# Kernel tuning notes

Hardware: AMD Instinct MI355X
Metric: run time of the kernel (lower is better)

## Reference

```python
import jax, jax.numpy as jnp
import numpy as np

B, S, H, NH, L, V, P = 2, 1024, 768, 12, 4, 32000, 1024
HD = H // NH  # head dim = 64; matches scale_val = hidden/num_heads


def setup_inputs() -> dict:
    key = jax.random.key(0)
    ks = jax.random.split(key, 18)
    sc = 0.02
    n = jax.random.normal
    return {
        "input_ids": jax.random.randint(ks[0], (B, S), 0, V, dtype=jnp.int32),
        "seq_mask": jnp.ones((B, S), jnp.float32),
        "bpe_emb": (n(ks[1], (V, H)) * sc).astype(jnp.float32),
        "pos_emb": (n(ks[2], (P, H)) * sc).astype(jnp.float32),
        "qkv_w": (n(ks[3], (L, H, 3 * H)) * sc).astype(jnp.float32),
        "qkv_b": jnp.zeros((L, 3 * H), jnp.float32),
        "res_w": (n(ks[4], (L, H, H)) * sc).astype(jnp.float32),
        "res_b": jnp.zeros((L, H), jnp.float32),
        "ln1_g": jnp.ones((L, H), jnp.float32),
        "ln1_b": jnp.zeros((L, H), jnp.float32),
        "ff1_w": (n(ks[5], (L, H, 4 * H)) * sc).astype(jnp.float32),
        "ff1_b": jnp.zeros((L, 4 * H), jnp.float32),
        "ff2_w": (n(ks[6], (L, 4 * H, H)) * sc).astype(jnp.float32),
        "ff2_b": jnp.zeros((L, H), jnp.float32),
        "ln2_g": jnp.ones((L, H), jnp.float32),
        "ln2_b": jnp.zeros((L, H), jnp.float32),
        "pred_w": (n(ks[7], (H, V)) * sc).astype(jnp.float32),
    }


def _layer_norm(x, g, b, e=1e-5):
    u = jnp.mean(x, -1, keepdims=True)
    s = jnp.mean((x - u) ** 2, -1, keepdims=True)
    return g * ((x - u) / jnp.sqrt(s + e)) + b


def _attention(x, seq_mask, w_qkv, b_qkv, w_res, b_res):
    qkv = x @ w_qkv + b_qkv                    # [B,S,3H]
    q, k, v = jnp.split(qkv, 3, axis=-1)
    q = q.reshape(B, S, NH, HD)
    k = k.reshape(B, S, NH, HD)
    v = v.reshape(B, S, NH, HD)
    score = jnp.einsum('bqhd,bkhd->bhqk', q, k) / jnp.sqrt(jnp.float32(HD))
    tril = jnp.tril(jnp.ones((S, S), jnp.float32))           # causal
    mask = tril[None, None] * seq_mask[:, None, None, :]      # [B,1,S,S]
    score = score + (1.0 - mask) * -1e9
    prob = jax.nn.softmax(score, axis=-1)      # dropout rate 0 -> identity
    val = jnp.einsum('bhqk,bkhd->bqhd', prob, v).reshape(B, S, H)
    return val @ w_res + b_res                 # dropout rate 0 -> identity


def reference(input_ids, seq_mask, bpe_emb, pos_emb, qkv_w, qkv_b, res_w, res_b,
              ln1_g, ln1_b, ff1_w, ff1_b, ff2_w, ff2_b, ln2_g, ln2_b, pred_w):
    pos_idx = jnp.arange(S)
    h = bpe_emb[input_ids] + pos_emb[pos_idx][None]           # [B,S,H]
    for l in range(L):
        a = _attention(h, seq_mask, qkv_w[l], qkv_b[l], res_w[l], res_b[l])
        h = _layer_norm(h + a, ln1_g[l], ln1_b[l])
        m = (jax.nn.gelu(h @ ff1_w[l] + ff1_b[l], approximate=False)
             @ ff2_w[l] + ff2_b[l])
        h = _layer_norm(h + m, ln2_g[l], ln2_b[l])
    pred_score = h @ pred_w                                   # [B,S,V]
    pred_prob = jax.nn.softmax(pred_score, axis=-1)
    return pred_score, pred_prob
```

## Files before the change

kernel.cpp:

```cpp
#include <hip/hip_runtime.h>
#include <math.h>

#define BB 2
#define SS 1024
#define HH 768
#define NHEAD 12
#define HDIM 64
#define NLAYER 4
#define VV 32000
#define MROWS (BB*SS)

typedef unsigned short u16;
typedef __attribute__((ext_vector_type(8))) short short8;
typedef __attribute__((ext_vector_type(4))) float f32x4;
typedef __attribute__((ext_vector_type(4))) unsigned short u16x4;

__device__ __forceinline__ u16 f2bf(float f) {
    union { float f; unsigned u; } x; x.f = f;
    unsigned r = (x.u + 0x7fff + ((x.u >> 16) & 1)) >> 16;
    return (u16)r;
}
__device__ __forceinline__ float bf2f(u16 b) {
    union { unsigned u; float f; } x; x.u = ((unsigned)b) << 16;
    return x.f;
}

__device__ __forceinline__ void gload_lds16(const u16* g, u16* l) {
    __builtin_amdgcn_global_load_lds((const __attribute__((address_space(1))) void*)g,
                                     (__attribute__((address_space(3))) void*)l, 16, 0, 0);
}

__global__ __launch_bounds__(256) void conv_all(
    const float* __restrict__ qkv_w, u16* __restrict__ qkvT,
    const float* __restrict__ res_w, u16* __restrict__ resT,
    const float* __restrict__ ff1_w, u16* __restrict__ ff1T,
    const float* __restrict__ ff2_w, u16* __restrict__ ff2T,
    const float* __restrict__ pred_w, u16* __restrict__ predT) {
    int id = blockIdx.x;
    const float* W; u16* Wt; int K, N, rem;
    if (id < 6912) {
        int l = id / 1728; rem = id - l * 1728;
        W = qkv_w + (size_t)l * HH * 3 * HH; Wt = qkvT + (size_t)l * HH * 3 * HH;
        K = HH; N = 3 * HH;
    } else if (id < 9216) {
        id -= 6912; int l = id / 576; rem = id - l * 576;
        W = res_w + (size_t)l * HH * HH; Wt = resT + (size_t)l * HH * HH;
        K = HH; N = HH;
    } else if (id < 18432) {
        id -= 9216; int l = id / 2304; rem = id - l * 2304;
        W = ff1_w + (size_t)l * HH * 4 * HH; Wt = ff1T + (size_t)l * HH * 4 * HH;
        K = HH; N = 4 * HH;
    } else if (id < 27648) {
        id -= 18432; int l = id / 2304; rem = id - l * 2304;
        W = ff2_w + (size_t)l * 4 * HH * HH; Wt = ff2T + (size_t)l * 4 * HH * HH;
        K = 4 * HH; N = HH;
    } else {
        rem = id - 27648;
        W = pred_w; Wt = predT; K = HH; N = VV;
    }
    const int nt = N / 32;
    const int k0 = (rem / nt) * 32, n0 = (rem % nt) * 32;

    __shared__ u16 tile[32][33];
    int t = threadIdx.x;
    int ky = t >> 3, nx = (t & 7) * 4;
    float4 v = *(const float4*)(W + (size_t)(k0 + ky) * N + n0 + nx);
    tile[nx + 0][ky] = f2bf(v.x);
    tile[nx + 1][ky] = f2bf(v.y);
    tile[nx + 2][ky] = f2bf(v.z);
    tile[nx + 3][ky] = f2bf(v.w);
    __syncthreads();
    int nr = t >> 3, kc = (t & 7) * 4;
    u16x4 o;
    o[0] = tile[nr][kc + 0]; o[1] = tile[nr][kc + 1];
    o[2] = tile[nr][kc + 2]; o[3] = tile[nr][kc + 3];
    *(u16x4*)(Wt + (size_t)(n0 + nr) * K + k0 + kc) = o;
}

__global__ void embed_kernel(const int* __restrict__ ids,
                             const float* __restrict__ bpe,
                             const float* __restrict__ pos,
                             float* __restrict__ h, u16* __restrict__ hb) {
    int row = blockIdx.x;
    int s = row % SS;
    int id = ids[row];
    const float4* br = (const float4*)(bpe + (size_t)id * HH);
    const float4* pr = (const float4*)(pos + (size_t)s * HH);
    float4* hr = (float4*)(h + (size_t)row * HH);
    u16x4* hbr = (u16x4*)(hb + (size_t)row * HH);
    int t = threadIdx.x;
    float4 a = br[t], c = pr[t];
    a.x += c.x; a.y += c.y; a.z += c.z; a.w += c.w;
    hr[t] = a;
    u16x4 u; u[0] = f2bf(a.x); u[1] = f2bf(a.y); u[2] = f2bf(a.z); u[3] = f2bf(a.w);
    hbr[t] = u;
}

template<int BM, int THREADS, int WN, int ACT, int WF32, int WBF>
__global__ __launch_bounds__(THREADS) void mfma_gemm(
    const u16* __restrict__ A, const u16* __restrict__ Wt,
    const float* __restrict__ bias, float* __restrict__ C,
    u16* __restrict__ Cb, int M, int N, int K) {
    constexpr int WM = THREADS / 64 / WN;
    constexpr int MR = BM / (WM * 16);
    constexpr int NR = 128 / (WN * 16);
    constexpr int LPT = (BM * 8 + 1024) / THREADS;
    __shared__ u16 As[2 * BM * 64];
    __shared__ u16 Bs[2 * 128 * 64];
    const int tid = threadIdx.x;
    const int lane = tid & 63;
    const int wid = tid >> 6;

    const int nwg = gridDim.x * gridDim.y;
    int id = blockIdx.x + gridDim.x * blockIdx.y;
    int id2 = (nwg & 7) ? id : ((id & 7) * (nwg >> 3) + (id >> 3));
    const int brow = (id2 % gridDim.x) * BM;
    const int bcol = (id2 / gridDim.x) * 128;

    const int wr = (wid / WN) * (MR * 16);
    const int wc = (wid % WN) * (NR * 16);
    f32x4 acc[MR][NR] = {};

    const u16* Abase = A + (size_t)brow * K;
    const u16* Bbase = Wt + (size_t)bcol * K;
    const int lrow = lane & 15;
    const int lhi = lane >> 4;

    auto stage = [&](u16* Ad, u16* Bd, int kt) {
#pragma unroll
        for (int c0 = 0; c0 < BM * 8; c0 += THREADS) {
            int c = c0 + tid;
            int r = c >> 3, s = c & 7;
            gload_lds16(Abase + (size_t)r * K + kt + ((s ^ (r & 7)) * 8), Ad + c * 8);
        }
#pragma unroll
        for (int c0 = 0; c0 < 1024; c0 += THREADS) {
            int c = c0 + tid;
            int r = c >> 3, s = c & 7;
            gload_lds16(Bbase + (size_t)r * K + kt + ((s ^ (r & 7)) * 8), Bd + c * 8);
        }
    };

    const int nt = K / 64;
    stage(As, Bs, 0);
    for (int t = 0; t < nt; ++t) {
        u16* Ac = As + (t & 1) * (BM * 64);
        u16* Bc = Bs + (t & 1) * (128 * 64);
        if (t + 1 < nt) {
            stage(As + ((t + 1) & 1) * (BM * 64),
                  Bs + ((t + 1) & 1) * (128 * 64), (t + 1) * 64);
            if constexpr (LPT == 8)      asm volatile("s_waitcnt vmcnt(8)" ::: "memory");
            else if constexpr (LPT == 6) asm volatile("s_waitcnt vmcnt(6)" ::: "memory");
            else if constexpr (LPT == 5) asm volatile("s_waitcnt vmcnt(5)" ::: "memory");
            else                         asm volatile("s_waitcnt vmcnt(4)" ::: "memory");
        } else {
            asm volatile("s_waitcnt vmcnt(0)" ::: "memory");
        }
        __builtin_amdgcn_s_barrier();
        __builtin_amdgcn_sched_barrier(0);

        short8 a[MR][2], b[NR][2];
#pragma unroll
        for (int m = 0; m < MR; ++m) {
            const int R = wr + m * 16 + lrow;
            char* rp = (char*)Ac + R * 128;
#pragma unroll
            for (int kk = 0; kk < 2; ++kk)
                a[m][kk] = *(const short8*)(rp + (((kk * 4 + lhi) ^ (R & 7)) * 16));
        }
#pragma unroll
        for (int n = 0; n < NR; ++n) {
            const int R = wc + n * 16 + lrow;
            char* rp = (char*)Bc + R * 128;
#pragma unroll
            for (int kk = 0; kk < 2; ++kk)
                b[n][kk] = *(const short8*)(rp + (((kk * 4 + lhi) ^ (R & 7)) * 16));
        }
        __builtin_amdgcn_s_setprio(1);
#pragma unroll
        for (int kk = 0; kk < 2; ++kk)
#pragma unroll
            for (int m = 0; m < MR; ++m)
#pragma unroll
                for (int n = 0; n < NR; ++n)
                    acc[m][n] = __builtin_amdgcn_mfma_f32_16x16x32_bf16(a[m][kk], b[n][kk], acc[m][n], 0, 0, 0);
        __builtin_amdgcn_s_setprio(0);

        __builtin_amdgcn_sched_barrier(0);
        __builtin_amdgcn_s_barrier();
    }

    const int lr4 = (lane >> 4) * 4;
#pragma unroll
    for (int n = 0; n < NR; ++n) {
        int col = bcol + wc + n * 16 + lrow;
        float bv = bias ? bias[col] : 0.f;
#pragma unroll
        for (int m = 0; m < MR; ++m) {
#pragma unroll
            for (int j = 0; j < 4; ++j) {
                int row = brow + wr + m * 16 + lr4 + j;
                float v = acc[m][n][j] + bv;
                if (ACT == 1) v = 0.5f * v * (1.f + erff(v * 0.70710678118654752f));
                if (WF32) C[(size_t)row * N + col] = v;
                if (WBF)  Cb[(size_t)row * N + col] = f2bf(v);
            }
        }
    }
}

__global__ __launch_bounds__(256) void attn_kernel(
    const u16* __restrict__ qkvb, const float* __restrict__ seq_mask,
    u16* __restrict__ av) {
    __shared__ u16 Ks[128 * 64];
    __shared__ u16 Vt[64 * 128];
    __shared__ u16 Ps[64 * 128];
    const int qb = gridDim.x - 1 - blockIdx.x;
    const int hd = blockIdx.y, b = blockIdx.z;
    const int t = threadIdx.x;
    const int lane = t & 63;
    const int w = t >> 6;
    const int lrow = lane & 15;
    const int lhi = lane >> 4;
    const int q0 = qb * 64;
    const size_t rs = 3 * HH;

    short8 aq[2];
    {
        const u16* qrow = qkvb + (size_t)(b * SS + q0 + w * 16 + lrow) * rs + hd * HDIM;
        aq[0] = *(const short8*)(qrow + lhi * 8);
        aq[1] = *(const short8*)(qrow + 32 + lhi * 8);
    }

    f32x4 o[4] = {};
    float m_[4] = {-INFINITY, -INFINITY, -INFINITY, -INFINITY};
    float l_[4] = {0.f, 0.f, 0.f, 0.f};

    const int kr = t >> 1;
    const int ch = t & 1;
    const int ntile = (q0 + 64 + 127) / 128;

    short8 kR[4], vR[4];
    {
        const u16* kbase = qkvb + (size_t)(b * SS + kr) * rs + HH + hd * HDIM + ch * 32;
#pragma unroll
        for (int i = 0; i < 4; ++i) {
            kR[i] = *(const short8*)(kbase + i * 8);
            vR[i] = *(const short8*)(kbase + HH + i * 8);
        }
    }

    for (int kt = 0; kt < ntile; ++kt) {
        const int k0 = kt * 128;
        __syncthreads();
        {
            char* kp = (char*)Ks + kr * 128;
#pragma unroll
            for (int i = 0; i < 4; ++i)
                *(short8*)(kp + (((ch * 4 + i) ^ (kr & 7)) << 4)) = kR[i];
            const int vslot = kr >> 3;
            const int voff = (kr & 7) * 2;
#pragma unroll
            for (int i = 0; i < 4; ++i)
#pragma unroll
                for (int e = 0; e < 8; ++e) {
                    int d = ch * 32 + i * 8 + e;
                    *(u16*)((char*)Vt + d * 256 + ((vslot ^ (d & 15)) << 4) + voff) = (u16)vR[i][e];
                }
        }
        __syncthreads();

        if (kt + 1 < ntile) {
            const u16* kbase = qkvb + (size_t)(b * SS + k0 + 128 + kr) * rs + HH + hd * HDIM + ch * 32;
#pragma unroll
            for (int i = 0; i < 4; ++i) {
                kR[i] = *(const short8*)(kbase + i * 8);
                vR[i] = *(const short8*)(kbase + HH + i * 8);
            }
        }

        f32x4 s[8] = {};
        __builtin_amdgcn_s_setprio(1);
#pragma unroll
        for (int n = 0; n < 8; ++n) {
            const int krow = n * 16 + lrow;
            char* kp = (char*)Ks + krow * 128;
#pragma unroll
            for (int c = 0; c < 2; ++c) {
                short8 bk = *(const short8*)(kp + (((c * 4 + lhi) ^ (krow & 7)) << 4));
                s[n] = __builtin_amdgcn_mfma_f32_16x16x32_bf16(aq[c], bk, s[n], 0, 0, 0);
            }
        }
        __builtin_amdgcn_s_setprio(0);

        float sm[8];
#pragma unroll
        for (int n = 0; n < 8; ++n) sm[n] = seq_mask[b * SS + k0 + n * 16 + lrow];
        const int diag = (kt == ntile - 1);
#pragma unroll
        for (int j = 0; j < 4; ++j) {
            const int qglob = q0 + w * 16 + lhi * 4 + j;
            float sv[8];
#pragma unroll
            for (int n = 0; n < 8; ++n) {
                const int kglob = k0 + n * 16 + lrow;
                float msk = (diag && kglob > qglob) ? 0.f : sm[n];
                sv[n] = s[n][j] * 0.125f + (1.f - msk) * (-1e9f);
            }
            float tm = fmaxf(fmaxf(fmaxf(sv[0], sv[1]), fmaxf(sv[2], sv[3])),
                             fmaxf(fmaxf(sv[4], sv[5]), fmaxf(sv[6], sv[7])));
            tm = fmaxf(tm, __shfl_xor(tm, 1));
            tm = fmaxf(tm, __shfl_xor(tm, 2));
            tm = fmaxf(tm, __shfl_xor(tm, 4));
            tm = fmaxf(tm, __shfl_xor(tm, 8));
            float mn = fmaxf(m_[j], tm);
            float sc = __expf(m_[j] - mn);
            float ps = 0.f;
#pragma unroll
            for (int n = 0; n < 8; ++n) {
                float p = __expf(sv[n] - mn);
                s[n][j] = p;
                ps += p;
            }
            ps += __shfl_xor(ps, 1);
            ps += __shfl_xor(ps, 2);
            ps += __shfl_xor(ps, 4);
            ps += __shfl_xor(ps, 8);
            l_[j] = l_[j] * sc + ps;
            m_[j] = mn;
#pragma unroll
            for (int dn = 0; dn < 4; ++dn) o[dn][j] *= sc;
        }

#pragma unroll
        for (int j = 0; j < 4; ++j) {
            const int prow = w * 16 + lhi * 4 + j;
            char* pp = (char*)Ps + prow * 256;
            const int poff = (lrow & 7) * 2;
#pragma unroll
            for (int n = 0; n < 8; ++n) {
                int slot = 2 * n + (lrow >> 3);
                *(u16*)(pp + ((slot ^ (prow & 15)) << 4) + poff) = f2bf(s[n][j]);
            }
        }

        const int arow = w * 16 + lrow;
        char* ap_p = (char*)Ps + arow * 256;
        __builtin_amdgcn_s_setprio(1);
#pragma unroll
        for (int c = 0; c < 4; ++c) {
            short8 ap = *(const short8*)(ap_p + (((c * 4 + lhi) ^ (arow & 15)) << 4));
#pragma unroll
            for (int dn = 0; dn < 4; ++dn) {
                const int vrow = dn * 16 + lrow;
                short8 bv = *(const short8*)((char*)Vt + vrow * 256 +
                                             (((c * 4 + lhi) ^ (vrow & 15)) << 4));
                o[dn] = __builtin_amdgcn_mfma_f32_16x16x32_bf16(ap, bv, o[dn], 0, 0, 0);
            }
        }
        __builtin_amdgcn_s_setprio(0);
    }

#pragma unroll
    for (int j = 0; j < 4; ++j) {
        const int q = q0 + w * 16 + lhi * 4 + j;
        const float inv = 1.f / l_[j];
        u16* orow = av + (size_t)(b * SS + q) * HH + hd * HDIM;
#pragma unroll
        for (int dn = 0; dn < 4; ++dn)
            orow[dn * 16 + lrow] = f2bf(o[dn][j] * inv);
    }
}

__global__ __launch_bounds__(256) void add_ln_kernel(
    float* __restrict__ h, u16* __restrict__ hb,
    const u16* __restrict__ ab,
    const float* __restrict__ g, const float* __restrict__ bta) {
    const int row = blockIdx.x * 4 + (threadIdx.x >> 6);
    const int lane = threadIdx.x & 63;
    const size_t base = (size_t)row * HH;

    float x[12];
    float sum = 0.f;
#pragma unroll
    for (int c = 0; c < 3; ++c) {
        const int col = lane * 4 + c * 256;
        float4 hv = *(const float4*)(h + base + col);
        u16x4 av = *(const u16x4*)(ab + base + col);
        x[c*4+0] = hv.x + bf2f(av[0]);
        x[c*4+1] = hv.y + bf2f(av[1]);
        x[c*4+2] = hv.z + bf2f(av[2]);
        x[c*4+3] = hv.w + bf2f(av[3]);
        sum += x[c*4+0] + x[c*4+1] + x[c*4+2] + x[c*4+3];
    }
#pragma unroll
    for (int off = 32; off; off >>= 1) sum += __shfl_xor(sum, off);
    const float mean = sum * (1.0f / 768.0f);

    float vs = 0.f;
#pragma unroll
    for (int e = 0; e < 12; ++e) { float d = x[e] - mean; vs += d * d; }
#pragma unroll
    for (int off = 32; off; off >>= 1) vs += __shfl_xor(vs, off);
    const float inv = 1.0f / sqrtf(vs * (1.0f / 768.0f) + 1e-5f);

#pragma unroll
    for (int c = 0; c < 3; ++c) {
        const int col = lane * 4 + c * 256;
        float4 gv = *(const float4*)(g + col);
        float4 bv = *(const float4*)(bta + col);
        float y0 = gv.x * (x[c*4+0] - mean) * inv + bv.x;
        float y1 = gv.y * (x[c*4+1] - mean) * inv + bv.y;
        float y2 = gv.z * (x[c*4+2] - mean) * inv + bv.z;
        float y3 = gv.w * (x[c*4+3] - mean) * inv + bv.w;
        float4 hv; hv.x = y0; hv.y = y1; hv.z = y2; hv.w = y3;
        *(float4*)(h + base + col) = hv;
        u16x4 u; u[0] = f2bf(y0); u[1] = f2bf(y1); u[2] = f2bf(y2); u[3] = f2bf(y3);
        *(u16x4*)(hb + base + col) = u;
    }
}

__global__ __launch_bounds__(512) void softmax_v_kernel(
    const float* __restrict__ score, float* __restrict__ prob) {
    __shared__ u16 srow[VV];
    __shared__ float red[512];
    int row = blockIdx.x;
    int t = threadIdx.x;
    const float4* sr = (const float4*)(score + (size_t)row * VV);
    float4* pr = (float4*)(prob + (size_t)row * VV);
    const int n4 = VV / 4;

    float mx = -INFINITY;
    for (int i = t; i < n4; i += 512) {
        float4 v = sr[i];
        u16x4 u; u[0] = f2bf(v.x); u[1] = f2bf(v.y); u[2] = f2bf(v.z); u[3] = f2bf(v.w);
        *(u16x4*)(srow + i * 4) = u;
        mx = fmaxf(mx, fmaxf(fmaxf(bf2f(u[0]), bf2f(u[1])), fmaxf(bf2f(u[2]), bf2f(u[3]))));
    }
    red[t] = mx; __syncthreads();
    for (int o = 256; o; o >>= 1) { if (t < o) red[t] = fmaxf(red[t], red[t + o]); __syncthreads(); }
    mx = red[0];
    __syncthreads();

    float s = 0.f;
    for (int i = t; i < n4; i += 512) {
        u16x4 u = *(const u16x4*)(srow + i * 4);
        s += __expf(bf2f(u[0]) - mx) + __expf(bf2f(u[1]) - mx)
           + __expf(bf2f(u[2]) - mx) + __expf(bf2f(u[3]) - mx);
    }
    red[t] = s; __syncthreads();
    for (int o = 256; o; o >>= 1) { if (t < o) red[t] += red[t + o]; __syncthreads(); }
    float inv = 1.0f / red[0];

    for (int i = t; i < n4; i += 512) {
        u16x4 u = *(const u16x4*)(srow + i * 4);
        float4 o4;
        o4.x = __expf(bf2f(u[0]) - mx) * inv; o4.y = __expf(bf2f(u[1]) - mx) * inv;
        o4.z = __expf(bf2f(u[2]) - mx) * inv; o4.w = __expf(bf2f(u[3]) - mx) * inv;
        pr[i] = o4;
    }
}

extern "C" void kernel_launch(void* const* d_in, const int* in_sizes, int n_in,
                              void* d_out, int out_size, void* d_ws, size_t ws_size,
                              hipStream_t stream) {
    const int*   ids      = (const int*)d_in[0];
    const float* seq_mask = (const float*)d_in[1];
    const float* bpe      = (const float*)d_in[2];
    const float* pos      = (const float*)d_in[3];
    const float* qkv_w    = (const float*)d_in[4];
    const float* qkv_b    = (const float*)d_in[5];
    const float* res_w    = (const float*)d_in[6];
    const float* res_b    = (const float*)d_in[7];
    const float* ln1_g    = (const float*)d_in[8];
    const float* ln1_b    = (const float*)d_in[9];
    const float* ff1_w    = (const float*)d_in[10];
    const float* ff1_b    = (const float*)d_in[11];
    const float* ff2_w    = (const float*)d_in[12];
    const float* ff2_b    = (const float*)d_in[13];
    const float* ln2_g    = (const float*)d_in[14];
    const float* ln2_b    = (const float*)d_in[15];
    const float* pred_w   = (const float*)d_in[16];

    float* out_score = (float*)d_out;
    float* out_prob  = out_score + (size_t)MROWS * VV;

    size_t off = 0;
    auto take = [&](size_t bytes) -> size_t {
        size_t p = off; off += (bytes + 255) & ~(size_t)255; return p;
    };
    const size_t o_qkvT = take((size_t)NLAYER * HH * 3 * HH * 2);
    const size_t o_resT = take((size_t)NLAYER * HH * HH * 2);
    const size_t o_ff1T = take((size_t)NLAYER * HH * 4 * HH * 2);
    const size_t o_ff2T = take((size_t)NLAYER * 4 * HH * HH * 2);
    const size_t o_predT = take((size_t)HH * VV * 2);
    const size_t o_h    = take((size_t)MROWS * HH * 4);
    const size_t o_ab   = take((size_t)MROWS * HH * 2);
    const size_t o_qkvb = take((size_t)MROWS * 3 * HH * 2);
    const size_t o_hb   = take((size_t)MROWS * HH * 2);
    const size_t o_avb  = take((size_t)MROWS * HH * 2);
    const size_t o_midb = take((size_t)MROWS * 4 * HH * 2);
    const size_t need = off;

    char* arena = (ws_size >= need) ? (char*)d_ws : (char*)out_prob;
    u16*   qkvT = (u16*)(arena + o_qkvT);
    u16*   resT = (u16*)(arena + o_resT);
    u16*   ff1T = (u16*)(arena + o_ff1T);
    u16*   ff2T = (u16*)(arena + o_ff2T);
    u16*   predT = (u16*)(arena + o_predT);
    float* h    = (float*)(arena + o_h);
    u16*   ab   = (u16*)(arena + o_ab);
    u16*   qkvb = (u16*)(arena + o_qkvb);
    u16*   hb   = (u16*)(arena + o_hb);
    u16*   avb  = (u16*)(arena + o_avb);
    u16*   midb = (u16*)(arena + o_midb);

    conv_all<<<51648, 256, 0, stream>>>(qkv_w, qkvT, res_w, resT,
                                        ff1_w, ff1T, ff2_w, ff2T, pred_w, predT);

    embed_kernel<<<MROWS, 192, 0, stream>>>(ids, bpe, pos, h, hb);

    for (int l = 0; l < NLAYER; ++l) {
        mfma_gemm<64, 256, 2, 0, 0, 1><<<dim3(MROWS / 64, 3 * HH / 128), 256, 0, stream>>>(
            hb, qkvT + (size_t)l * HH * 3 * HH, qkv_b + (size_t)l * 3 * HH,
            nullptr, qkvb, MROWS, 3 * HH, HH);
        attn_kernel<<<dim3(SS / 64, NHEAD, BB), 256, 0, stream>>>(qkvb, seq_mask, avb);
        mfma_gemm<32, 256, 2, 0, 0, 1><<<dim3(MROWS / 32, HH / 128), 256, 0, stream>>>(
            avb, resT + (size_t)l * HH * HH, res_b + (size_t)l * HH,
            nullptr, ab, MROWS, HH, HH);
        add_ln_kernel<<<MROWS / 4, 256, 0, stream>>>(h, hb, ab,
            ln1_g + (size_t)l * HH, ln1_b + (size_t)l * HH);
        mfma_gemm<64, 256, 2, 1, 0, 1><<<dim3(MROWS / 64, 4 * HH / 128), 256, 0, stream>>>(
            hb, ff1T + (size_t)l * HH * 4 * HH, ff1_b + (size_t)l * 4 * HH,
            nullptr, midb, MROWS, 4 * HH, HH);
        mfma_gemm<32, 256, 2, 0, 0, 1><<<dim3(MROWS / 32, HH / 128), 256, 0, stream>>>(
            midb, ff2T + (size_t)l * 4 * HH * HH, ff2_b + (size_t)l * HH,
            nullptr, ab, MROWS, HH, 4 * HH);
        add_ln_kernel<<<MROWS / 4, 256, 0, stream>>>(h, hb, ab,
            ln2_g + (size_t)l * HH, ln2_b + (size_t)l * HH);
    }

    mfma_gemm<128, 512, 4, 0, 1, 0><<<dim3(MROWS / 128, VV / 128), 512, 0, stream>>>(
        hb, predT, nullptr, out_score, nullptr, MROWS, VV, HH);
    softmax_v_kernel<<<MROWS, 512, 0, stream>>>(out_score, out_prob);
}
```

Measured before the change: 933.9 us.

## Generalize GEMM to multi-stage pipeline with configurable K-tile depth

```diff
diff --git a/kernel.cpp b/kernel.cpp
--- a/kernel.cpp
+++ b/kernel.cpp
@@ -96,7 +96,7 @@
     hbr[t] = u;
 }
 
-template<int BM, int THREADS, int WN, int ACT, int WF32, int WBF>
+template<int BM, int BK, int NBUF, int THREADS, int WN, int ACT, int WF32, int WBF>
 __global__ __launch_bounds__(THREADS) void mfma_gemm(
     const u16* __restrict__ A, const u16* __restrict__ Wt,
     const float* __restrict__ bias, float* __restrict__ C,
@@ -104,9 +104,15 @@
     constexpr int WM = THREADS / 64 / WN;
     constexpr int MR = BM / (WM * 16);
     constexpr int NR = 128 / (WN * 16);
-    constexpr int LPT = (BM * 8 + 1024) / THREADS;
-    __shared__ u16 As[2 * BM * 64];
-    __shared__ u16 Bs[2 * 128 * 64];
+    constexpr int KK = BK / 32;
+    constexpr int SLOTS = BK / 8;
+    constexpr int SM = SLOTS - 1;
+    constexpr int RB = BK * 2;
+    constexpr int ACH = BM * BK / 8;
+    constexpr int BCH = 128 * BK / 8;
+    constexpr int LPT = (ACH + BCH) / THREADS;
+    __shared__ u16 As[NBUF * BM * BK];
+    __shared__ u16 Bs[NBUF * 128 * BK];
     const int tid = threadIdx.x;
     const int lane = tid & 63;
     const int wid = tid >> 6;
@@ -126,59 +132,72 @@
     const int lrow = lane & 15;
     const int lhi = lane >> 4;
 
-    auto stage = [&](u16* Ad, u16* Bd, int kt) {
-#pragma unroll
-        for (int c0 = 0; c0 < BM * 8; c0 += THREADS) {
+    auto stage = [&](int buf, int tile) {
+        const int kt = tile * BK;
+        u16* Ad = As + buf * (BM * BK);
+        u16* Bd = Bs + buf * (128 * BK);
+#pragma unroll
+        for (int c0 = 0; c0 < ACH; c0 += THREADS) {
             int c = c0 + tid;
-            int r = c >> 3, s = c & 7;
-            gload_lds16(Abase + (size_t)r * K + kt + ((s ^ (r & 7)) * 8), Ad + c * 8);
-        }
-#pragma unroll
-        for (int c0 = 0; c0 < 1024; c0 += THREADS) {
+            int r = c / SLOTS, s = c & SM;
+            gload_lds16(Abase + (size_t)r * K + kt + ((s ^ (r & SM)) * 8), Ad + c * 8);
+        }
+#pragma unroll
+        for (int c0 = 0; c0 < BCH; c0 += THREADS) {
             int c = c0 + tid;
-            int r = c >> 3, s = c & 7;
-            gload_lds16(Bbase + (size_t)r * K + kt + ((s ^ (r & 7)) * 8), Bd + c * 8);
+            int r = c / SLOTS, s = c & SM;
+            gload_lds16(Bbase + (size_t)r * K + kt + ((s ^ (r & SM)) * 8), Bd + c * 8);
         }
     };
 
-    const int nt = K / 64;
-    stage(As, Bs, 0);
+    const int nt = K / BK;
+#pragma unroll
+    for (int p = 0; p < NBUF - 1; ++p)
+        if (p < nt) stage(p, p);
+
     for (int t = 0; t < nt; ++t) {
-        u16* Ac = As + (t & 1) * (BM * 64);
-        u16* Bc = Bs + (t & 1) * (128 * 64);
-        if (t + 1 < nt) {
-            stage(As + ((t + 1) & 1) * (BM * 64),
-                  Bs + ((t + 1) & 1) * (128 * 64), (t + 1) * 64);
-            if constexpr (LPT == 8)      asm volatile("s_waitcnt vmcnt(8)" ::: "memory");
-            else if constexpr (LPT == 6) asm volatile("s_waitcnt vmcnt(6)" ::: "memory");
+        const int nf = t + NBUF - 1;
+        if (nf < nt) stage(nf % NBUF, nf);
+        const int rem = ((nf < nt) ? nf : (nt - 1)) - t;
+        if (rem <= 0) {
+            asm volatile("s_waitcnt vmcnt(0)" ::: "memory");
+        } else if (rem == 1) {
+            if constexpr (LPT == 3)      asm volatile("s_waitcnt vmcnt(3)" ::: "memory");
+            else if constexpr (LPT == 4) asm volatile("s_waitcnt vmcnt(4)" ::: "memory");
             else if constexpr (LPT == 5) asm volatile("s_waitcnt vmcnt(5)" ::: "memory");
-            else                         asm volatile("s_waitcnt vmcnt(4)" ::: "memory");
+            else                         asm volatile("s_waitcnt vmcnt(6)" ::: "memory");
+        } else if (rem == 2) {
+            if constexpr (LPT == 3)      asm volatile("s_waitcnt vmcnt(6)" ::: "memory");
+            else                         asm volatile("s_waitcnt vmcnt(12)" ::: "memory");
         } else {
-            asm volatile("s_waitcnt vmcnt(0)" ::: "memory");
+            if constexpr (LPT == 3)      asm volatile("s_waitcnt vmcnt(9)" ::: "memory");
+            else                         asm volatile("s_waitcnt vmcnt(18)" ::: "memory");
         }
         __builtin_amdgcn_s_barrier();
         __builtin_amdgcn_sched_barrier(0);
 
-        short8 a[MR][2], b[NR][2];
+        u16* Ac = As + (t % NBUF) * (BM * BK);
+        u16* Bc = Bs + (t % NBUF) * (128 * BK);
+        short8 a[MR][KK], b[NR][KK];
 #pragma unroll
         for (int m = 0; m < MR; ++m) {
             const int R = wr + m * 16 + lrow;
-            char* rp = (char*)Ac + R * 128;
-#pragma unroll
-            for (int kk = 0; kk < 2; ++kk)
-                a[m][kk] = *(const short8*)(rp + (((kk * 4 + lhi) ^ (R & 7)) * 16));
+            char* rp = (char*)Ac + R * RB;
+#pragma unroll
+            for (int kk = 0; kk < KK; ++kk)
+                a[m][kk] = *(const short8*)(rp + (((kk * 4 + lhi) ^ (R & SM)) * 16));
         }
 #pragma unroll
         for (int n = 0; n < NR; ++n) {
             const int R = wc + n * 16 + lrow;
-            char* rp = (char*)Bc + R * 128;
-#pragma unroll
-            for (int kk = 0; kk < 2; ++kk)
-                b[n][kk] = *(const short8*)(rp + (((kk * 4 + lhi) ^ (R & 7)) * 16));
+            char* rp = (char*)Bc + R * RB;
+#pragma unroll
+            for (int kk = 0; kk < KK; ++kk)
+                b[n][kk] = *(const short8*)(rp + (((kk * 4 + lhi) ^ (R & SM)) * 16));
         }
         __builtin_amdgcn_s_setprio(1);
 #pragma unroll
-        for (int kk = 0; kk < 2; ++kk)
+        for (int kk = 0; kk < KK; ++kk)
 #pragma unroll
             for (int m = 0; m < MR; ++m)
 #pragma unroll
@@ -521,26 +540,26 @@
     embed_kernel<<<MROWS, 192, 0, stream>>>(ids, bpe, pos, h, hb);
 
     for (int l = 0; l < NLAYER; ++l) {
-        mfma_gemm<64, 256, 2, 0, 0, 1><<<dim3(MROWS / 64, 3 * HH / 128), 256, 0, stream>>>(
+        mfma_gemm<64, 32, 4, 256, 2, 0, 0, 1><<<dim3(MROWS / 64, 3 * HH / 128), 256, 0, stream>>>(
             hb, qkvT + (size_t)l * HH * 3 * HH, qkv_b + (size_t)l * 3 * HH,
             nullptr, qkvb, MROWS, 3 * HH, HH);
         attn_kernel<<<dim3(SS / 64, NHEAD, BB), 256, 0, stream>>>(qkvb, seq_mask, avb);
-        mfma_gemm<32, 256, 2, 0, 0, 1><<<dim3(MROWS / 32, HH / 128), 256, 0, stream>>>(
+        mfma_gemm<32, 64, 2, 256, 2, 0, 0, 1><<<dim3(MROWS / 32, HH / 128), 256, 0, stream>>>(
             avb, resT + (size_t)l * HH * HH, res_b + (size_t)l * HH,
             nullptr, ab, MROWS, HH, HH);
         add_ln_kernel<<<MROWS / 4, 256, 0, stream>>>(h, hb, ab,
             ln1_g + (size_t)l * HH, ln1_b + (size_t)l * HH);
-        mfma_gemm<64, 256, 2, 1, 0, 1><<<dim3(MROWS / 64, 4 * HH / 128), 256, 0, stream>>>(
+        mfma_gemm<64, 32, 4, 256, 2, 1, 0, 1><<<dim3(MROWS / 64, 4 * HH / 128), 256, 0, stream>>>(
             hb, ff1T + (size_t)l * HH * 4 * HH, ff1_b + (size_t)l * 4 * HH,
             nullptr, midb, MROWS, 4 * HH, HH);
-        mfma_gemm<32, 256, 2, 0, 0, 1><<<dim3(MROWS / 32, HH / 128), 256, 0, stream>>>(
+        mfma_gemm<32, 64, 2, 256, 2, 0, 0, 1><<<dim3(MROWS / 32, HH / 128), 256, 0, stream>>>(
             midb, ff2T + (size_t)l * 4 * HH * HH, ff2_b + (size_t)l * HH,
             nullptr, ab, MROWS, HH, 4 * HH);
         add_ln_kernel<<<MROWS / 4, 256, 0, stream>>>(h, hb, ab,
             ln2_g + (size_t)l * HH, ln2_b + (size_t)l * HH);
     }
 
-    mfma_gemm<128, 512, 4, 0, 1, 0><<<dim3(MROWS / 128, VV / 128), 512, 0, stream>>>(
+    mfma_gemm<128, 64, 2, 512, 4, 0, 1, 0><<<dim3(MROWS / 128, VV / 128), 512, 0, stream>>>(
         hb, predT, nullptr, out_score, nullptr, MROWS, VV, HH);
     softmax_v_kernel<<<MROWS, 512, 0, stream>>>(out_score, out_prob);
 }
```

New measurement: 959.1 us. 2.7% more time.

## Split attention KV range across two blocks and merge partials in a combine kernel

Applied to the files above, without the earlier changes.

```diff
diff --git a/kernel.cpp b/kernel.cpp
--- a/kernel.cpp
+++ b/kernel.cpp
@@ -35,8 +35,26 @@
     const float* __restrict__ res_w, u16* __restrict__ resT,
     const float* __restrict__ ff1_w, u16* __restrict__ ff1T,
     const float* __restrict__ ff2_w, u16* __restrict__ ff2T,
-    const float* __restrict__ pred_w, u16* __restrict__ predT) {
+    const float* __restrict__ pred_w, u16* __restrict__ predT,
+    const int* __restrict__ ids, const float* __restrict__ bpe,
+    const float* __restrict__ pos, float* __restrict__ h, u16* __restrict__ hb) {
     int id = blockIdx.x;
+    if (id >= 51648) {
+        int row = id - 51648;
+        int t = threadIdx.x;
+        if (t < 192) {
+            int s = row % SS;
+            int tok = ids[row];
+            const float4* br = (const float4*)(bpe + (size_t)tok * HH);
+            const float4* pr = (const float4*)(pos + (size_t)s * HH);
+            float4 a = br[t], c = pr[t];
+            a.x += c.x; a.y += c.y; a.z += c.z; a.w += c.w;
+            ((float4*)(h + (size_t)row * HH))[t] = a;
+            u16x4 u; u[0] = f2bf(a.x); u[1] = f2bf(a.y); u[2] = f2bf(a.z); u[3] = f2bf(a.w);
+            ((u16x4*)(hb + (size_t)row * HH))[t] = u;
+        }
+        return;
+    }
     const float* W; u16* Wt; int K, N, rem;
     if (id < 6912) {
         int l = id / 1728; rem = id - l * 1728;
@@ -77,25 +95,6 @@
     *(u16x4*)(Wt + (size_t)(n0 + nr) * K + k0 + kc) = o;
 }
 
-__global__ void embed_kernel(const int* __restrict__ ids,
-                             const float* __restrict__ bpe,
-                             const float* __restrict__ pos,
-                             float* __restrict__ h, u16* __restrict__ hb) {
-    int row = blockIdx.x;
-    int s = row % SS;
-    int id = ids[row];
-    const float4* br = (const float4*)(bpe + (size_t)id * HH);
-    const float4* pr = (const float4*)(pos + (size_t)s * HH);
-    float4* hr = (float4*)(h + (size_t)row * HH);
-    u16x4* hbr = (u16x4*)(hb + (size_t)row * HH);
-    int t = threadIdx.x;
-    float4 a = br[t], c = pr[t];
-    a.x += c.x; a.y += c.y; a.z += c.z; a.w += c.w;
-    hr[t] = a;
-    u16x4 u; u[0] = f2bf(a.x); u[1] = f2bf(a.y); u[2] = f2bf(a.z); u[3] = f2bf(a.w);
-    hbr[t] = u;
-}
-
 template<int BM, int THREADS, int WN, int ACT, int WF32, int WBF>
 __global__ __launch_bounds__(THREADS) void mfma_gemm(
     const u16* __restrict__ A, const u16* __restrict__ Wt,
@@ -211,11 +210,12 @@
 
 __global__ __launch_bounds__(256) void attn_kernel(
     const u16* __restrict__ qkvb, const float* __restrict__ seq_mask,
-    u16* __restrict__ av) {
+    float* __restrict__ Opart, float2* __restrict__ ml) {
     __shared__ u16 Ks[128 * 64];
     __shared__ u16 Vt[64 * 128];
     __shared__ u16 Ps[64 * 128];
-    const int qb = gridDim.x - 1 - blockIdx.x;
+    const int qb = (gridDim.x >> 1) - 1 - (blockIdx.x >> 1);
+    const int sp = blockIdx.x & 1;
     const int hd = blockIdx.y, b = blockIdx.z;
     const int t = threadIdx.x;
     const int lane = t & 63;
@@ -225,6 +225,11 @@
     const int q0 = qb * 64;
     const size_t rs = 3 * HH;
 
+    const int ntile = (q0 + 64 + 127) / 128;
+    const int half = (ntile + 1) >> 1;
+    const int kbeg = sp ? half : 0;
+    const int kend = sp ? ntile : half;
+
     short8 aq[2];
     {
         const u16* qrow = qkvb + (size_t)(b * SS + q0 + w * 16 + lrow) * rs + hd * HDIM;
@@ -238,11 +243,10 @@
 
     const int kr = t >> 1;
     const int ch = t & 1;
-    const int ntile = (q0 + 64 + 127) / 128;
 
     short8 kR[4], vR[4];
-    {
-        const u16* kbase = qkvb + (size_t)(b * SS + kr) * rs + HH + hd * HDIM + ch * 32;
+    if (kbeg < kend) {
+        const u16* kbase = qkvb + (size_t)(b * SS + kbeg * 128 + kr) * rs + HH + hd * HDIM + ch * 32;
 #pragma unroll
         for (int i = 0; i < 4; ++i) {
             kR[i] = *(const short8*)(kbase + i * 8);
@@ -250,7 +254,7 @@
         }
     }
 
-    for (int kt = 0; kt < ntile; ++kt) {
+    for (int kt = kbeg; kt < kend; ++kt) {
         const int k0 = kt * 128;
         __syncthreads();
         {
@@ -270,7 +274,7 @@
         }
         __syncthreads();
 
-        if (kt + 1 < ntile) {
+        if (kt + 1 < kend) {
             const u16* kbase = qkvb + (size_t)(b * SS + k0 + 128 + kr) * rs + HH + hd * HDIM + ch * 32;
 #pragma unroll
             for (int i = 0; i < 4; ++i) {
@@ -361,15 +365,35 @@
         __builtin_amdgcn_s_setprio(0);
     }
 
+    float* obase = Opart + (size_t)sp * MROWS * HH;
 #pragma unroll
     for (int j = 0; j < 4; ++j) {
         const int q = q0 + w * 16 + lhi * 4 + j;
-        const float inv = 1.f / l_[j];
-        u16* orow = av + (size_t)(b * SS + q) * HH + hd * HDIM;
+        float* orow = obase + (size_t)(b * SS + q) * HH + hd * HDIM;
 #pragma unroll
         for (int dn = 0; dn < 4; ++dn)
-            orow[dn * 16 + lrow] = f2bf(o[dn][j] * inv);
-    }
+            orow[dn * 16 + lrow] = o[dn][j];
+        if (lrow == 0) {
+            float2 v; v.x = m_[j]; v.y = l_[j];
+            ml[((size_t)sp * MROWS + b * SS + q) * NHEAD + hd] = v;
+        }
+    }
+}
+
+__global__ __launch_bounds__(768) void attn_combine(
+    const float* __restrict__ Opart, const float2* __restrict__ ml,
+    u16* __restrict__ av) {
+    const int row = blockIdx.x;
+    const int t = threadIdx.x;
+    const int hd = t >> 6;
+    float2 a1 = ml[(size_t)row * NHEAD + hd];
+    float2 a2 = ml[((size_t)MROWS + row) * NHEAD + hd];
+    float m = fmaxf(a1.x, a2.x);
+    float c1 = __expf(a1.x - m), c2 = __expf(a2.x - m);
+    float inv = 1.f / (a1.y * c1 + a2.y * c2);
+    float o1 = Opart[(size_t)row * HH + t];
+    float o2 = Opart[(size_t)(MROWS + row) * HH + t];
+    av[(size_t)row * HH + t] = f2bf((o1 * c1 + o2 * c2) * inv);
 }
 
 __global__ __launch_bounds__(256) void add_ln_kernel(
@@ -500,6 +524,8 @@
     const size_t o_hb   = take((size_t)MROWS * HH * 2);
     const size_t o_avb  = take((size_t)MROWS * HH * 2);
     const size_t o_midb = take((size_t)MROWS * 4 * HH * 2);
+    const size_t o_op   = take((size_t)2 * MROWS * HH * 4);
+    const size_t o_ml   = take((size_t)2 * MROWS * NHEAD * 8);
     const size_t need = off;
 
     char* arena = (ws_size >= need) ? (char*)d_ws : (char*)out_prob;
@@ -514,17 +540,19 @@
     u16*   hb   = (u16*)(arena + o_hb);
     u16*   avb  = (u16*)(arena + o_avb);
     u16*   midb = (u16*)(arena + o_midb);
-
-    conv_all<<<51648, 256, 0, stream>>>(qkv_w, qkvT, res_w, resT,
-                                        ff1_w, ff1T, ff2_w, ff2T, pred_w, predT);
-
-    embed_kernel<<<MROWS, 192, 0, stream>>>(ids, bpe, pos, h, hb);
+    float* opart = (float*)(arena + o_op);
+    float2* mlb  = (float2*)(arena + o_ml);
+
+    conv_all<<<53696, 256, 0, stream>>>(qkv_w, qkvT, res_w, resT,
+                                        ff1_w, ff1T, ff2_w, ff2T, pred_w, predT,
+                                        ids, bpe, pos, h, hb);
 
     for (int l = 0; l < NLAYER; ++l) {
         mfma_gemm<64, 256, 2, 0, 0, 1><<<dim3(MROWS / 64, 3 * HH / 128), 256, 0, stream>>>(
             hb, qkvT + (size_t)l * HH * 3 * HH, qkv_b + (size_t)l * 3 * HH,
             nullptr, qkvb, MROWS, 3 * HH, HH);
-        attn_kernel<<<dim3(SS / 64, NHEAD, BB), 256, 0, stream>>>(qkvb, seq_mask, avb);
+        attn_kernel<<<dim3(SS / 64 * 2, NHEAD, BB), 256, 0, stream>>>(qkvb, seq_mask, opart, mlb);
+        attn_combine<<<MROWS, 768, 0, stream>>>(opart, mlb, avb);
         mfma_gemm<32, 256, 2, 0, 0, 1><<<dim3(MROWS / 32, HH / 128), 256, 0, stream>>>(
             avb, resT + (size_t)l * HH * HH, res_b + (size_t)l * HH,
             nullptr, ab, MROWS, HH, HH);
```

Result: no change. 952.5 us (+2.0%).
